# Kernel optimization log

Hardware: AMD Instinct MI355X
Metric: run time of the kernel (lower is better)

Reference implementation:

```python
import jax, jax.numpy as jnp
import numpy as np

VOCAB = 32000
HIDDEN = 512
T = 1024


def setup_inputs() -> dict:
    key = jax.random.key(0)
    ks = jax.random.split(key, 8)
    s = 0.05  # weight scale so tanh does not fully saturate
    return {
        "inputs_idxs": jax.random.randint(ks[0], (T,), 0, VOCAB),
        "h": jax.random.normal(ks[1], (1, HIDDEN), dtype=jnp.float32),
        "Wxh_w": jax.random.normal(ks[2], (HIDDEN, VOCAB), dtype=jnp.float32) * s,
        "Wxh_b": jax.random.normal(ks[3], (HIDDEN,), dtype=jnp.float32) * s,
        "Whh_w": jax.random.normal(ks[4], (HIDDEN, HIDDEN), dtype=jnp.float32) * s,
        "Whh_b": jax.random.normal(ks[5], (HIDDEN,), dtype=jnp.float32) * s,
        "Why_w": jax.random.normal(ks[6], (VOCAB, HIDDEN), dtype=jnp.float32) * s,
        "Why_b": jax.random.normal(ks[7], (VOCAB,), dtype=jnp.float32) * s,
    }


def reference(inputs_idxs, h, Wxh_w, Wxh_b, Whh_w, Whh_b, Why_w, Why_b):
    # Teacher forcing: one-hot(inputs[t]) @ Wxh_w.T == gather column inputs[t]
    xh = Wxh_w[:, inputs_idxs].T + Wxh_b  # (T, hidden)

    def step(h_prev, xh_t):
        h_new = jnp.tanh(xh_t + h_prev @ Whh_w.T + Whh_b)  # (hidden,)
        return h_new, h_new

    h_final, h_seq = jax.lax.scan(step, h[0], xh)  # h_seq: (T, hidden)
    logits = h_seq @ Why_w.T + Why_b  # (T, vocab) -- one big GEMM
    return logits, h_final[None, :]
```

## Files before the change

### kernel.cpp

```cpp
#include <hip/hip_runtime.h>
#include <hip/hip_bf16.h>
#include <stdint.h>

#define VOCAB 32000
#define HIDDEN 512
#define TSEQ 1024
#define NWAVE 32
#define SENT 0x7F807F80u

typedef __attribute__((ext_vector_type(4))) float f32x4;
typedef __attribute__((ext_vector_type(8))) short short8;
typedef __attribute__((ext_vector_type(2))) unsigned uint2v;

union bfpack8 { short8 s; __hip_bfloat16 e[8]; };
union frag_u { short8 s; uint4 u; };

__global__ __launch_bounds__(256) void k_fill(uint4* __restrict__ p, int n4) {
  const int i = blockIdx.x * blockDim.x + threadIdx.x;
  if (i < n4) {
    uint4 v; v.x = SENT; v.y = SENT; v.z = SENT; v.w = SENT;
    p[i] = v;
  }
}

__global__ __launch_bounds__(256) void k_convert(const float* __restrict__ in,
                                                 __hip_bfloat16* __restrict__ out,
                                                 int n4) {
  int stride = gridDim.x * blockDim.x;
  for (int i = blockIdx.x * blockDim.x + threadIdx.x; i < n4; i += stride) {
    const float4 v = *reinterpret_cast<const float4*>(in + (size_t)i * 4);
    union { __hip_bfloat16 h[4]; ushort4 u; } p;
    p.h[0] = __float2bfloat16(v.x);
    p.h[1] = __float2bfloat16(v.y);
    p.h[2] = __float2bfloat16(v.z);
    p.h[3] = __float2bfloat16(v.w);
    *reinterpret_cast<ushort4*>(out + (size_t)i * 4) = p.u;
  }
}

__global__ __launch_bounds__(512) void k_pre(const int* __restrict__ idx,
                                             const float* __restrict__ h0,
                                             const float* __restrict__ Wxh_w,
                                             const float* __restrict__ Wxh_b,
                                             const float* __restrict__ Whh_b,
                                             float* __restrict__ pre,
                                             __hip_bfloat16* __restrict__ h_bf) {
  const int t = blockIdx.x;
  const int j = threadIdx.x;
  const int c = idx[t];
  pre[(size_t)t * HIDDEN + j] = Wxh_w[(size_t)j * VOCAB + c] + Wxh_b[j] + Whh_b[j];
  if (t == 0) h_bf[j] = __float2bfloat16(h0[j]);
}

__global__ __launch_bounds__(64, 1) void k_scan(const float* __restrict__ pre,
                                                const float* __restrict__ Whh,
                                                __hip_bfloat16* __restrict__ h_bf,
                                                float* __restrict__ h_final) {
  __shared__ short8 afrag[32][64];
  __shared__ __align__(16) __hip_bfloat16 hstage[HIDDEN];

  const int wv = blockIdx.x;
  const int l = threadIdx.x;
  const int l15 = l & 15;
  const int l4 = l >> 4;
  const int base = wv * 16;

  {
    const float* wp = Whh + (size_t)(base + l15) * HIDDEN + l4 * 8;
#pragma unroll
    for (int kk = 0; kk < 16; ++kk) {
      const f32x4 a = *reinterpret_cast<const f32x4*>(wp + kk * 32);
      const f32x4 b = *reinterpret_cast<const f32x4*>(wp + kk * 32 + 4);
      bfpack8 hi, lo;
#pragma unroll
      for (int i = 0; i < 4; ++i) {
        hi.e[i] = __float2bfloat16(a[i]);
        lo.e[i] = __float2bfloat16(a[i] - __bfloat162float(hi.e[i]));
        hi.e[4 + i] = __float2bfloat16(b[i]);
        lo.e[4 + i] = __float2bfloat16(b[i] - __bfloat162float(hi.e[4 + i]));
      }
      afrag[2 * kk][l] = hi.s;
      afrag[2 * kk + 1][l] = lo.s;
    }
  }

  for (int t = 1; t <= TSEQ; ++t) {
    const float* pp = pre + (size_t)(t - 1) * HIDDEN + base + l4 * 4;
    const f32x4 pv = *reinterpret_cast<const f32x4*>(pp);

    const __hip_bfloat16* hrow = h_bf + (size_t)(t - 1) * HIDDEN + l * 8;
    short8 hv;
    unsigned ok;
    do {
      asm volatile("global_load_dwordx4 %0, %1, off sc0 sc1\n\ts_waitcnt vmcnt(0)"
                   : "=&v"(hv) : "v"(hrow) : "memory");
      frag_u f; f.s = hv;
      ok = (unsigned)(f.u.x != SENT) & (unsigned)(f.u.y != SENT) &
           (unsigned)(f.u.z != SENT) & (unsigned)(f.u.w != SENT);
    } while (!__all(ok != 0u));

    *reinterpret_cast<short8*>(&hstage[l * 8]) = hv;
    short8 bq[16];
#pragma unroll
    for (int kk = 0; kk < 16; ++kk)
      bq[kk] = *reinterpret_cast<const short8*>(&hstage[kk * 32 + l4 * 8]);

    f32x4 acc0 = {0.f, 0.f, 0.f, 0.f};
    f32x4 acc1 = {0.f, 0.f, 0.f, 0.f};
    f32x4 acc2 = {0.f, 0.f, 0.f, 0.f};
    f32x4 acc3 = {0.f, 0.f, 0.f, 0.f};
#pragma unroll
    for (int kk = 0; kk < 8; ++kk) {
      acc0 = __builtin_amdgcn_mfma_f32_16x16x32_bf16(afrag[2 * kk][l], bq[kk], acc0, 0, 0, 0);
      acc2 = __builtin_amdgcn_mfma_f32_16x16x32_bf16(afrag[2 * kk + 1][l], bq[kk], acc2, 0, 0, 0);
      acc1 = __builtin_amdgcn_mfma_f32_16x16x32_bf16(afrag[2 * (kk + 8)][l], bq[kk + 8], acc1, 0, 0, 0);
      acc3 = __builtin_amdgcn_mfma_f32_16x16x32_bf16(afrag[2 * (kk + 8) + 1][l], bq[kk + 8], acc3, 0, 0, 0);
    }
    const f32x4 acc = (acc0 + acc1) + (acc2 + acc3);

    float y[4];
#pragma unroll
    for (int q = 0; q < 4; ++q) {
      const float x = fminf(fmaxf(pv[q] + acc[q], -15.f), 15.f);
      const float e = __expf(2.f * x);
      y[q] = (e - 1.f) * __builtin_amdgcn_rcpf(e + 1.f);
    }

    if (l15 == 0) {
      union { uint2v u; __hip_bfloat16 e[4]; } pk;
#pragma unroll
      for (int q = 0; q < 4; ++q) pk.e[q] = __float2bfloat16(y[q]);
      __hip_bfloat16* ha = h_bf + (size_t)t * HIDDEN + base + l4 * 4;
      asm volatile("global_store_dwordx2 %0, %1, off sc0 sc1"
                   :: "v"(ha), "v"(pk.u) : "memory");
      if (t == TSEQ) {
        f32x4 f = {y[0], y[1], y[2], y[3]};
        *reinterpret_cast<f32x4*>(h_final + base + l4 * 4) = f;
      }
    }
  }
}

__global__ __launch_bounds__(256) void k_gemm(const __hip_bfloat16* __restrict__ A,
                                              const __hip_bfloat16* __restrict__ B,
                                              const float* __restrict__ bias,
                                              float* __restrict__ C) {
  __shared__ __hip_bfloat16 As[128][32];
  __shared__ __hip_bfloat16 Bs[128][32];
  const int bn = blockIdx.x;
  const int bm = blockIdx.y;
  const int tid = threadIdx.x;
  const int lane = tid & 63;
  const int wid = tid >> 6;
  const int wr = (wid >> 1) * 64;
  const int wc = (wid & 1) * 64;
  const int l15 = lane & 15;
  const int kc = lane >> 4;

  const int sr = tid >> 1;
  const int sc = (tid & 1) * 16;

  const __hip_bfloat16* Ag = A + (size_t)(bm * 128 + sr) * HIDDEN + sc;
  const __hip_bfloat16* Bg = B + (size_t)(bn * 128 + sr) * HIDDEN + sc;

  f32x4 acc[4][4];
#pragma unroll
  for (int m = 0; m < 4; ++m)
#pragma unroll
    for (int n = 0; n < 4; ++n) {
      acc[m][n][0] = 0.f; acc[m][n][1] = 0.f; acc[m][n][2] = 0.f; acc[m][n][3] = 0.f;
    }

  for (int ks = 0; ks < HIDDEN; ks += 32) {
    __syncthreads();
    *reinterpret_cast<short8*>(&As[sr][sc])     = *reinterpret_cast<const short8*>(Ag + ks);
    *reinterpret_cast<short8*>(&As[sr][sc + 8]) = *reinterpret_cast<const short8*>(Ag + ks + 8);
    *reinterpret_cast<short8*>(&Bs[sr][sc])     = *reinterpret_cast<const short8*>(Bg + ks);
    *reinterpret_cast<short8*>(&Bs[sr][sc + 8]) = *reinterpret_cast<const short8*>(Bg + ks + 8);
    __syncthreads();

    short8 af[4], bfr[4];
#pragma unroll
    for (int m = 0; m < 4; ++m)
      af[m] = *reinterpret_cast<const short8*>(&As[wr + m * 16 + l15][kc * 8]);
#pragma unroll
    for (int n = 0; n < 4; ++n)
      bfr[n] = *reinterpret_cast<const short8*>(&Bs[wc + n * 16 + l15][kc * 8]);
#pragma unroll
    for (int m = 0; m < 4; ++m)
#pragma unroll
      for (int n = 0; n < 4; ++n)
        acc[m][n] = __builtin_amdgcn_mfma_f32_16x16x32_bf16(af[m], bfr[n], acc[m][n], 0, 0, 0);
  }

#pragma unroll
  for (int m = 0; m < 4; ++m) {
#pragma unroll
    for (int n = 0; n < 4; ++n) {
      const int vcol = bn * 128 + wc + n * 16 + l15;
      const float bv = bias[vcol];
#pragma unroll
      for (int q = 0; q < 4; ++q) {
        const int trow = bm * 128 + wr + m * 16 + kc * 4 + q;
        C[(size_t)trow * VOCAB + vcol] = acc[m][n][q] + bv;
      }
    }
  }
}

extern "C" void kernel_launch(void* const* d_in, const int* in_sizes, int n_in,
                              void* d_out, int out_size, void* d_ws, size_t ws_size,
                              hipStream_t stream) {
  (void)in_sizes; (void)n_in; (void)out_size; (void)ws_size;

  const int*   idx   = (const int*)d_in[0];
  const float* h0    = (const float*)d_in[1];
  const float* Wxh_w = (const float*)d_in[2];
  const float* Wxh_b = (const float*)d_in[3];
  const float* Whh_w = (const float*)d_in[4];
  const float* Whh_b = (const float*)d_in[5];
  const float* Why_w = (const float*)d_in[6];
  const float* Why_b = (const float*)d_in[7];
  float* out = (float*)d_out;

  char* ws = (char*)d_ws;
  __hip_bfloat16* why_bf = (__hip_bfloat16*)(ws);
  float* pre = (float*)(ws + 32768000);
  __hip_bfloat16* h_bf = (__hip_bfloat16*)(ws + 32768000 + 2097152);

  k_fill<<<(TSEQ * HIDDEN / 8 + 255) / 256, 256, 0, stream>>>(
      (uint4*)(h_bf + HIDDEN), TSEQ * HIDDEN / 8);
  k_convert<<<2048, 256, 0, stream>>>(Why_w, why_bf, (VOCAB * HIDDEN) / 4);
  k_pre<<<TSEQ, HIDDEN, 0, stream>>>(idx, h0, Wxh_w, Wxh_b, Whh_b, pre, h_bf);
  k_scan<<<NWAVE, 64, 0, stream>>>(pre, Whh_w, h_bf, out + 32768000);
  k_gemm<<<dim3(VOCAB / 128, TSEQ / 128), 256, 0, stream>>>(h_bf + HIDDEN, why_bf, Why_b, out);
}
```

Baseline: 1.516 ms.

## Fuse scan and output GEMM into one persistent kernel overlapping via sentinel polling

Merges the recurrent scan and the logits GEMM into a single persistent launch: 32 blocks run the scan while the remaining 224 blocks process GEMM tiles, each tile waiting (by polling sentinel values in h_bf) until the 128 timesteps it needs are produced. The separate Why_w fp32->bf16 conversion pass is removed and the conversion is done inline while loading B tiles. The goal is to hide the GEMM behind the long serial scan and to skip an extra pass over the weight matrix. In exchange, every tile reloads and reconverts fp32 weights, and the design depends on all 256 blocks being co-resident, otherwise it deadlocks; polling also uses memory bandwidth.

```diff
diff --git a/kernel.cpp b/kernel.cpp
--- a/kernel.cpp
+++ b/kernel.cpp
@@ -5,8 +5,11 @@
 #define VOCAB 32000
 #define HIDDEN 512
 #define TSEQ 1024
-#define NWAVE 32
 #define SENT 0x7F807F80u
+#define NSCANBLK 32
+#define NBLK 256
+#define NGEMMBLK (NBLK - NSCANBLK)
+#define NTILE 2000
 
 typedef __attribute__((ext_vector_type(4))) float f32x4;
 typedef __attribute__((ext_vector_type(8))) short short8;
@@ -20,21 +23,6 @@
   if (i < n4) {
     uint4 v; v.x = SENT; v.y = SENT; v.z = SENT; v.w = SENT;
     p[i] = v;
-  }
-}
-
-__global__ __launch_bounds__(256) void k_convert(const float* __restrict__ in,
-                                                 __hip_bfloat16* __restrict__ out,
-                                                 int n4) {
-  int stride = gridDim.x * blockDim.x;
-  for (int i = blockIdx.x * blockDim.x + threadIdx.x; i < n4; i += stride) {
-    const float4 v = *reinterpret_cast<const float4*>(in + (size_t)i * 4);
-    union { __hip_bfloat16 h[4]; ushort4 u; } p;
-    p.h[0] = __float2bfloat16(v.x);
-    p.h[1] = __float2bfloat16(v.y);
-    p.h[2] = __float2bfloat16(v.z);
-    p.h[3] = __float2bfloat16(v.w);
-    *reinterpret_cast<ushort4*>(out + (size_t)i * 4) = p.u;
   }
 }
 
@@ -52,159 +40,207 @@
   if (t == 0) h_bf[j] = __float2bfloat16(h0[j]);
 }
 
-__global__ __launch_bounds__(64, 1) void k_scan(const float* __restrict__ pre,
-                                                const float* __restrict__ Whh,
-                                                __hip_bfloat16* __restrict__ h_bf,
-                                                float* __restrict__ h_final) {
-  __shared__ short8 afrag[32][64];
-  __shared__ __align__(16) __hip_bfloat16 hstage[HIDDEN];
-
-  const int wv = blockIdx.x;
-  const int l = threadIdx.x;
-  const int l15 = l & 15;
-  const int l4 = l >> 4;
-  const int base = wv * 16;
-
-  {
-    const float* wp = Whh + (size_t)(base + l15) * HIDDEN + l4 * 8;
-#pragma unroll
-    for (int kk = 0; kk < 16; ++kk) {
-      const f32x4 a = *reinterpret_cast<const f32x4*>(wp + kk * 32);
-      const f32x4 b = *reinterpret_cast<const f32x4*>(wp + kk * 32 + 4);
-      bfpack8 hi, lo;
-#pragma unroll
-      for (int i = 0; i < 4; ++i) {
-        hi.e[i] = __float2bfloat16(a[i]);
-        lo.e[i] = __float2bfloat16(a[i] - __bfloat162float(hi.e[i]));
-        hi.e[4 + i] = __float2bfloat16(b[i]);
-        lo.e[4 + i] = __float2bfloat16(b[i] - __bfloat162float(hi.e[4 + i]));
-      }
-      afrag[2 * kk][l] = hi.s;
-      afrag[2 * kk + 1][l] = lo.s;
-    }
-  }
-
-  for (int t = 1; t <= TSEQ; ++t) {
-    const float* pp = pre + (size_t)(t - 1) * HIDDEN + base + l4 * 4;
-    const f32x4 pv = *reinterpret_cast<const f32x4*>(pp);
-
-    const __hip_bfloat16* hrow = h_bf + (size_t)(t - 1) * HIDDEN + l * 8;
-    short8 hv;
-    unsigned ok;
-    do {
-      asm volatile("global_load_dwordx4 %0, %1, off sc0 sc1\n\ts_waitcnt vmcnt(0)"
-                   : "=&v"(hv) : "v"(hrow) : "memory");
-      frag_u f; f.s = hv;
-      ok = (unsigned)(f.u.x != SENT) & (unsigned)(f.u.y != SENT) &
-           (unsigned)(f.u.z != SENT) & (unsigned)(f.u.w != SENT);
-    } while (!__all(ok != 0u));
-
-    *reinterpret_cast<short8*>(&hstage[l * 8]) = hv;
-    short8 bq[16];
-#pragma unroll
-    for (int kk = 0; kk < 16; ++kk)
-      bq[kk] = *reinterpret_cast<const short8*>(&hstage[kk * 32 + l4 * 8]);
-
-    f32x4 acc0 = {0.f, 0.f, 0.f, 0.f};
-    f32x4 acc1 = {0.f, 0.f, 0.f, 0.f};
-    f32x4 acc2 = {0.f, 0.f, 0.f, 0.f};
-    f32x4 acc3 = {0.f, 0.f, 0.f, 0.f};
-#pragma unroll
-    for (int kk = 0; kk < 8; ++kk) {
-      acc0 = __builtin_amdgcn_mfma_f32_16x16x32_bf16(afrag[2 * kk][l], bq[kk], acc0, 0, 0, 0);
-      acc2 = __builtin_amdgcn_mfma_f32_16x16x32_bf16(afrag[2 * kk + 1][l], bq[kk], acc2, 0, 0, 0);
-      acc1 = __builtin_amdgcn_mfma_f32_16x16x32_bf16(afrag[2 * (kk + 8)][l], bq[kk + 8], acc1, 0, 0, 0);
-      acc3 = __builtin_amdgcn_mfma_f32_16x16x32_bf16(afrag[2 * (kk + 8) + 1][l], bq[kk + 8], acc3, 0, 0, 0);
-    }
-    const f32x4 acc = (acc0 + acc1) + (acc2 + acc3);
-
-    float y[4];
-#pragma unroll
-    for (int q = 0; q < 4; ++q) {
-      const float x = fminf(fmaxf(pv[q] + acc[q], -15.f), 15.f);
-      const float e = __expf(2.f * x);
-      y[q] = (e - 1.f) * __builtin_amdgcn_rcpf(e + 1.f);
-    }
-
-    if (l15 == 0) {
-      union { uint2v u; __hip_bfloat16 e[4]; } pk;
-#pragma unroll
-      for (int q = 0; q < 4; ++q) pk.e[q] = __float2bfloat16(y[q]);
-      __hip_bfloat16* ha = h_bf + (size_t)t * HIDDEN + base + l4 * 4;
-      asm volatile("global_store_dwordx2 %0, %1, off sc0 sc1"
-                   :: "v"(ha), "v"(pk.u) : "memory");
-      if (t == TSEQ) {
-        f32x4 f = {y[0], y[1], y[2], y[3]};
-        *reinterpret_cast<f32x4*>(h_final + base + l4 * 4) = f;
-      }
-    }
-  }
-}
-
-__global__ __launch_bounds__(256) void k_gemm(const __hip_bfloat16* __restrict__ A,
-                                              const __hip_bfloat16* __restrict__ B,
-                                              const float* __restrict__ bias,
-                                              float* __restrict__ C) {
-  __shared__ __hip_bfloat16 As[128][32];
-  __shared__ __hip_bfloat16 Bs[128][32];
-  const int bn = blockIdx.x;
-  const int bm = blockIdx.y;
+__device__ __forceinline__ short8 poll16(const void* p) {
+  short8 v;
+  for (;;) {
+    asm volatile("global_load_dwordx4 %0, %1, off sc0 sc1\n\ts_waitcnt vmcnt(0)"
+                 : "=v"(v) : "v"(p));
+    frag_u f; f.s = v;
+    if ((f.u.x != SENT) & (f.u.y != SENT) & (f.u.z != SENT) & (f.u.w != SENT))
+      return v;
+  }
+}
+
+__global__ __launch_bounds__(256, 1) void k_fused(
+    const float* __restrict__ pre, const float* __restrict__ Whh,
+    __hip_bfloat16* __restrict__ h_bf, float* __restrict__ h_final,
+    const float* __restrict__ Why_w, const float* __restrict__ Why_b,
+    float* __restrict__ C) {
+  __shared__ __align__(16) char sh[33792];
+
+  const int blk = blockIdx.x;
   const int tid = threadIdx.x;
+
+  if (blk < NSCANBLK) {
+    if (tid >= 64) return;
+    short8 (*afrag)[64] = reinterpret_cast<short8 (*)[64]>(sh);
+    __hip_bfloat16* hstage = reinterpret_cast<__hip_bfloat16*>(sh + 32768);
+
+    const int wv = blk;
+    const int l = tid;
+    const int l15 = l & 15;
+    const int l4 = l >> 4;
+    const int base = wv * 16;
+
+    {
+      const float* wp = Whh + (size_t)(base + l15) * HIDDEN + l4 * 8;
+#pragma unroll
+      for (int kk = 0; kk < 16; ++kk) {
+        const f32x4 a = *reinterpret_cast<const f32x4*>(wp + kk * 32);
+        const f32x4 b = *reinterpret_cast<const f32x4*>(wp + kk * 32 + 4);
+        bfpack8 hi, lo;
+#pragma unroll
+        for (int i = 0; i < 4; ++i) {
+          hi.e[i] = __float2bfloat16(a[i]);
+          lo.e[i] = __float2bfloat16(a[i] - __bfloat162float(hi.e[i]));
+          hi.e[4 + i] = __float2bfloat16(b[i]);
+          lo.e[4 + i] = __float2bfloat16(b[i] - __bfloat162float(hi.e[4 + i]));
+        }
+        afrag[2 * kk][l] = hi.s;
+        afrag[2 * kk + 1][l] = lo.s;
+      }
+    }
+
+    for (int t = 1; t <= TSEQ; ++t) {
+      const float* pp = pre + (size_t)(t - 1) * HIDDEN + base + l4 * 4;
+      const f32x4 pv = *reinterpret_cast<const f32x4*>(pp);
+
+      const __hip_bfloat16* hrow = h_bf + (size_t)(t - 1) * HIDDEN + l * 8;
+      short8 hv;
+      unsigned ok;
+      do {
+        asm volatile("global_load_dwordx4 %0, %1, off sc0 sc1\n\ts_waitcnt vmcnt(0)"
+                     : "=&v"(hv) : "v"(hrow) : "memory");
+        frag_u f; f.s = hv;
+        ok = (unsigned)(f.u.x != SENT) & (unsigned)(f.u.y != SENT) &
+             (unsigned)(f.u.z != SENT) & (unsigned)(f.u.w != SENT);
+      } while (!__all(ok != 0u));
+
+      *reinterpret_cast<short8*>(&hstage[l * 8]) = hv;
+      short8 bq[16];
+#pragma unroll
+      for (int kk = 0; kk < 16; ++kk)
+        bq[kk] = *reinterpret_cast<const short8*>(&hstage[kk * 32 + l4 * 8]);
+
+      f32x4 acc0 = {0.f, 0.f, 0.f, 0.f};
+      f32x4 acc1 = {0.f, 0.f, 0.f, 0.f};
+      f32x4 acc2 = {0.f, 0.f, 0.f, 0.f};
+      f32x4 acc3 = {0.f, 0.f, 0.f, 0.f};
+#pragma unroll
+      for (int kk = 0; kk < 8; ++kk) {
+        acc0 = __builtin_amdgcn_mfma_f32_16x16x32_bf16(afrag[2 * kk][l], bq[kk], acc0, 0, 0, 0);
+        acc2 = __builtin_amdgcn_mfma_f32_16x16x32_bf16(afrag[2 * kk + 1][l], bq[kk], acc2, 0, 0, 0);
+        acc1 = __builtin_amdgcn_mfma_f32_16x16x32_bf16(afrag[2 * (kk + 8)][l], bq[kk + 8], acc1, 0, 0, 0);
+        acc3 = __builtin_amdgcn_mfma_f32_16x16x32_bf16(afrag[2 * (kk + 8) + 1][l], bq[kk + 8], acc3, 0, 0, 0);
+      }
+      const f32x4 acc = (acc0 + acc1) + (acc2 + acc3);
+
+      float y[4];
+#pragma unroll
+      for (int q = 0; q < 4; ++q) {
+        const float x = fminf(fmaxf(pv[q] + acc[q], -15.f), 15.f);
+        const float e = __expf(2.f * x);
+        y[q] = (e - 1.f) * __builtin_amdgcn_rcpf(e + 1.f);
+      }
+
+      if (l15 == 0) {
+        union { uint2v u; __hip_bfloat16 e[4]; } pk;
+#pragma unroll
+        for (int q = 0; q < 4; ++q) pk.e[q] = __float2bfloat16(y[q]);
+        __hip_bfloat16* ha = h_bf + (size_t)t * HIDDEN + base + l4 * 4;
+        asm volatile("global_store_dwordx2 %0, %1, off sc0 sc1"
+                     :: "v"(ha), "v"(pk.u) : "memory");
+        if (t == TSEQ) {
+          const f32x4 fo = {y[0], y[1], y[2], y[3]};
+          *reinterpret_cast<f32x4*>(h_final + base + l4 * 4) = fo;
+        }
+      }
+    }
+    return;
+  }
+
+  __hip_bfloat16 (*As)[32] = reinterpret_cast<__hip_bfloat16 (*)[32]>(sh);
+  __hip_bfloat16 (*Bs)[32] = reinterpret_cast<__hip_bfloat16 (*)[32]>(sh + 8192);
+
   const int lane = tid & 63;
   const int wid = tid >> 6;
   const int wr = (wid >> 1) * 64;
   const int wc = (wid & 1) * 64;
-  const int l15 = lane & 15;
+  const int l15g = lane & 15;
   const int kc = lane >> 4;
-
   const int sr = tid >> 1;
   const int sc = (tid & 1) * 16;
-
-  const __hip_bfloat16* Ag = A + (size_t)(bm * 128 + sr) * HIDDEN + sc;
-  const __hip_bfloat16* Bg = B + (size_t)(bn * 128 + sr) * HIDDEN + sc;
-
-  f32x4 acc[4][4];
-#pragma unroll
-  for (int m = 0; m < 4; ++m)
-#pragma unroll
-    for (int n = 0; n < 4; ++n) {
-      acc[m][n][0] = 0.f; acc[m][n][1] = 0.f; acc[m][n][2] = 0.f; acc[m][n][3] = 0.f;
-    }
-
-  for (int ks = 0; ks < HIDDEN; ks += 32) {
+  const __hip_bfloat16* A = h_bf + HIDDEN;
+
+  for (int tile = blk - NSCANBLK; tile < NTILE; tile += NGEMMBLK) {
+    const int bm = tile / 250;
+    const int bn = tile % 250;
+
+    if (tid == 0) {
+      const int sg = (bm * 128 + 129 < TSEQ) ? (bm * 128 + 129) : TSEQ;
+      const unsigned* gp = reinterpret_cast<const unsigned*>(h_bf + (size_t)sg * HIDDEN);
+      for (;;) {
+        unsigned v;
+        asm volatile("global_load_dword %0, %1, off sc0 sc1\n\ts_waitcnt vmcnt(0)"
+                     : "=v"(v) : "v"(gp));
+        if (v != SENT) break;
+        asm volatile("s_sleep 16");
+      }
+    }
     __syncthreads();
-    *reinterpret_cast<short8*>(&As[sr][sc])     = *reinterpret_cast<const short8*>(Ag + ks);
-    *reinterpret_cast<short8*>(&As[sr][sc + 8]) = *reinterpret_cast<const short8*>(Ag + ks + 8);
-    *reinterpret_cast<short8*>(&Bs[sr][sc])     = *reinterpret_cast<const short8*>(Bg + ks);
-    *reinterpret_cast<short8*>(&Bs[sr][sc + 8]) = *reinterpret_cast<const short8*>(Bg + ks + 8);
+
+    const __hip_bfloat16* Ag = A + (size_t)(bm * 128 + sr) * HIDDEN + sc;
+    const float* BgF = Why_w + (size_t)(bn * 128 + sr) * HIDDEN + sc;
+
+    f32x4 acc[4][4];
+#pragma unroll
+    for (int m = 0; m < 4; ++m)
+#pragma unroll
+      for (int n = 0; n < 4; ++n) {
+        acc[m][n][0] = 0.f; acc[m][n][1] = 0.f; acc[m][n][2] = 0.f; acc[m][n][3] = 0.f;
+      }
+
+    for (int ks = 0; ks < HIDDEN; ks += 32) {
+      __syncthreads();
+      const short8 a0 = poll16(Ag + ks);
+      const short8 a1 = poll16(Ag + ks + 8);
+      *reinterpret_cast<short8*>(&As[sr][sc]) = a0;
+      *reinterpret_cast<short8*>(&As[sr][sc + 8]) = a1;
+      const float* bp = BgF + ks;
+      const f32x4 x0 = *reinterpret_cast<const f32x4*>(bp);
+      const f32x4 x1 = *reinterpret_cast<const f32x4*>(bp + 4);
+      const f32x4 x2 = *reinterpret_cast<const f32x4*>(bp + 8);
+      const f32x4 x3 = *reinterpret_cast<const f32x4*>(bp + 12);
+      bfpack8 q0, q1;
+#pragma unroll
+      for (int i = 0; i < 4; ++i) {
+        q0.e[i] = __float2bfloat16(x0[i]);
+        q0.e[4 + i] = __float2bfloat16(x1[i]);
+        q1.e[i] = __float2bfloat16(x2[i]);
+        q1.e[4 + i] = __float2bfloat16(x3[i]);
+      }
+      *reinterpret_cast<short8*>(&Bs[sr][sc]) = q0.s;
+      *reinterpret_cast<short8*>(&Bs[sr][sc + 8]) = q1.s;
+      __syncthreads();
+
+      short8 af[4], bfr[4];
+#pragma unroll
+      for (int m = 0; m < 4; ++m)
+        af[m] = *reinterpret_cast<const short8*>(&As[wr + m * 16 + l15g][kc * 8]);
+#pragma unroll
+      for (int n = 0; n < 4; ++n)
+        bfr[n] = *reinterpret_cast<const short8*>(&Bs[wc + n * 16 + l15g][kc * 8]);
+#pragma unroll
+      for (int m = 0; m < 4; ++m)
+#pragma unroll
+        for (int n = 0; n < 4; ++n)
+          acc[m][n] = __builtin_amdgcn_mfma_f32_16x16x32_bf16(af[m], bfr[n], acc[m][n], 0, 0, 0);
+    }
+
+#pragma unroll
+    for (int m = 0; m < 4; ++m) {
+#pragma unroll
+      for (int n = 0; n < 4; ++n) {
+        const int vcol = bn * 128 + wc + n * 16 + l15g;
+        const float bv = Why_b[vcol];
+#pragma unroll
+        for (int q = 0; q < 4; ++q) {
+          const int trow = bm * 128 + wr + m * 16 + kc * 4 + q;
+          C[(size_t)trow * VOCAB + vcol] = acc[m][n][q] + bv;
+        }
+      }
+    }
     __syncthreads();
-
-    short8 af[4], bfr[4];
-#pragma unroll
-    for (int m = 0; m < 4; ++m)
-      af[m] = *reinterpret_cast<const short8*>(&As[wr + m * 16 + l15][kc * 8]);
-#pragma unroll
-    for (int n = 0; n < 4; ++n)
-      bfr[n] = *reinterpret_cast<const short8*>(&Bs[wc + n * 16 + l15][kc * 8]);
-#pragma unroll
-    for (int m = 0; m < 4; ++m)
-#pragma unroll
-      for (int n = 0; n < 4; ++n)
-        acc[m][n] = __builtin_amdgcn_mfma_f32_16x16x32_bf16(af[m], bfr[n], acc[m][n], 0, 0, 0);
-  }
-
-#pragma unroll
-  for (int m = 0; m < 4; ++m) {
-#pragma unroll
-    for (int n = 0; n < 4; ++n) {
-      const int vcol = bn * 128 + wc + n * 16 + l15;
-      const float bv = bias[vcol];
-#pragma unroll
-      for (int q = 0; q < 4; ++q) {
-        const int trow = bm * 128 + wr + m * 16 + kc * 4 + q;
-        C[(size_t)trow * VOCAB + vcol] = acc[m][n][q] + bv;
-      }
-    }
   }
 }
 
@@ -224,14 +260,12 @@
   float* out = (float*)d_out;
 
   char* ws = (char*)d_ws;
-  __hip_bfloat16* why_bf = (__hip_bfloat16*)(ws);
-  float* pre = (float*)(ws + 32768000);
-  __hip_bfloat16* h_bf = (__hip_bfloat16*)(ws + 32768000 + 2097152);
+  float* pre = (float*)ws;
+  __hip_bfloat16* h_bf = (__hip_bfloat16*)(ws + 2097152);
 
   k_fill<<<(TSEQ * HIDDEN / 8 + 255) / 256, 256, 0, stream>>>(
       (uint4*)(h_bf + HIDDEN), TSEQ * HIDDEN / 8);
-  k_convert<<<2048, 256, 0, stream>>>(Why_w, why_bf, (VOCAB * HIDDEN) / 4);
   k_pre<<<TSEQ, HIDDEN, 0, stream>>>(idx, h0, Wxh_w, Wxh_b, Whh_b, pre, h_bf);
-  k_scan<<<NWAVE, 64, 0, stream>>>(pre, Whh_w, h_bf, out + 32768000);
-  k_gemm<<<dim3(VOCAB / 128, TSEQ / 128), 256, 0, stream>>>(h_bf + HIDDEN, why_bf, Why_b, out);
-}
+  k_fused<<<NBLK, 256, 0, stream>>>(pre, Whh_w, h_bf, out + 32768000,
+                                    Why_w, Why_b, out);
+}
```

Result: faster. 1.469 ms (-3.1%).
